# Kernel optimization log

Hardware: AMD Instinct MI355X
Metric: run time of the kernel (lower is better)

## Reference

```python
import jax, jax.numpy as jnp
import numpy as np

D_MODEL = 1024
D_STATE = 64


def setup_inputs() -> dict:
    key = jax.random.key(0)
    k_x, k_a, k_b, k_c, k_d = jax.random.split(key, 5)
    x = jax.random.normal(k_x, (4, 4096, D_MODEL), dtype=jnp.float32)
    # parameter init mirrors _init_parameters
    A_diag = jax.random.uniform(k_a, (D_STATE,), minval=-0.5, maxval=0.5, dtype=jnp.float32)
    def xavier(k, shape):
        fan_in, fan_out = shape
        limit = float(np.sqrt(6.0 / (fan_in + fan_out)))
        return jax.random.uniform(k, shape, minval=-limit, maxval=limit, dtype=jnp.float32)
    B = xavier(k_b, (D_MODEL, D_STATE))
    C = xavier(k_c, (D_STATE, D_MODEL))
    D = xavier(k_d, (D_MODEL, D_MODEL)) * 0.1
    return {"x": x, "A_diag": A_diag, "B": B, "C": C, "D": D}


def reference(x, A_diag, B, C, D):
    # h_t = sigmoid(A_diag) * h_{t-1} + x_t @ B ; y_t = h_t @ C + x_t @ D
    # dropout is identity in eval mode.
    a = jax.nn.sigmoid(A_diag)                      # [S_state]
    u = jnp.einsum('btd,ds->bts', x, B)             # precompute input drive [B,T,S]

    def step(h, u_t):                               # h: [B,S], u_t: [B,S]
        h = a * h + u_t
        return h, h

    h0 = jnp.zeros((x.shape[0], A_diag.shape[0]), dtype=x.dtype)
    _, hs = jax.lax.scan(step, h0, jnp.swapaxes(u, 0, 1))  # hs: [T,B,S]
    hs = jnp.swapaxes(hs, 0, 1)                            # [B,T,S]
    y = jnp.einsum('bts,sd->btd', hs, C) + jnp.einsum('btd,de->bte', x, D)
    return y
```

## Files before the change

### kernel.cpp

```cpp
#include <hip/hip_runtime.h>
#include <hip/hip_bf16.h>

using bf16x8 = __attribute__((ext_vector_type(8))) __bf16;
using f32x4  = __attribute__((ext_vector_type(4))) float;

#define MTOT   16384
#define DMODEL 1024
#define DSTATE 64
#define KBIG   1088

__device__ __forceinline__ ushort f2b(float f) {
  __hip_bfloat16 h = __float2bfloat16(f);
  return *reinterpret_cast<ushort*>(&h);
}

__device__ __forceinline__ void gld_lds16(const ushort* g, const char* l) {
  using gptr_t = const __attribute__((address_space(1))) uint32_t*;
  using lptr_t = __attribute__((address_space(3))) uint32_t*;
  __builtin_amdgcn_global_load_lds(
      reinterpret_cast<gptr_t>(reinterpret_cast<uintptr_t>(g)),
      reinterpret_cast<lptr_t>(static_cast<uint32_t>(reinterpret_cast<uintptr_t>(l))),
      16, 0, 0);
}

#define BARRIER() do { asm volatile("" ::: "memory"); __builtin_amdgcn_s_barrier(); asm volatile("" ::: "memory"); } while (0)
#define VMCNT4() asm volatile("s_waitcnt vmcnt(4)" ::: "memory")
#define VMCNT0() asm volatile("s_waitcnt vmcnt(0)" ::: "memory")

__global__ void prep_params(const float* __restrict__ A_diag, const float* __restrict__ B,
                            const float* __restrict__ C, const float* __restrict__ D,
                            ushort* __restrict__ Wt, ushort* __restrict__ Btu,
                            float* __restrict__ aSig) {
  int i = blockIdx.x * blockDim.x + threadIdx.x;
  int stride = gridDim.x * blockDim.x;
  for (int idx = i; idx < DMODEL * KBIG; idx += stride) {
    int n = idx / KBIG, k = idx % KBIG;
    float v = (k < DSTATE) ? C[k * DMODEL + n] : D[(size_t)(k - DSTATE) * DMODEL + n];
    Wt[idx] = f2b(v);
  }
  for (int idx = i; idx < DSTATE * DMODEL; idx += stride) {
    int s = idx >> 10, k = idx & 1023;
    Btu[idx] = f2b(B[k * DSTATE + s]);
  }
  if (i < DSTATE) aSig[i] = 1.0f / (1.0f + expf(-A_diag[i]));
}

__global__ __launch_bounds__(256) void fused_xu(const float* __restrict__ x,
    const ushort* __restrict__ Btu, const float* __restrict__ aSig,
    ushort* __restrict__ Z, float* __restrict__ Uloc, float* __restrict__ carry) {
  __shared__ ushort As[64][136];
  __shared__ float  Ul[64][68];
  int tid = threadIdx.x;
  int w = tid >> 6, lane = tid & 63;
  int l16 = lane & 15, lh = lane >> 4;
  int row0 = blockIdx.x * 64;

  f32x4 acc[4] = {};
  float4 xv[4][2];
#pragma unroll
  for (int p = 0; p < 4; ++p) {
    int fi = p * 256 + tid;
    int r = fi >> 4, kq = fi & 15;
    const float* src = x + (size_t)(row0 + r) * 1024 + kq * 8;
    xv[p][0] = *reinterpret_cast<const float4*>(src);
    xv[p][1] = *reinterpret_cast<const float4*>(src + 4);
  }
  for (int c = 0; c < 8; ++c) {
    int k0 = c * 128;
#pragma unroll
    for (int p = 0; p < 4; ++p) {
      int fi = p * 256 + tid;
      int r = fi >> 4, kq = fi & 15;
      ushort o[8] = {f2b(xv[p][0].x), f2b(xv[p][0].y), f2b(xv[p][0].z), f2b(xv[p][0].w),
                     f2b(xv[p][1].x), f2b(xv[p][1].y), f2b(xv[p][1].z), f2b(xv[p][1].w)};
      uint4 pk = *reinterpret_cast<uint4*>(o);
      *reinterpret_cast<uint4*>(&Z[(size_t)(row0 + r) * KBIG + DSTATE + k0 + kq * 8]) = pk;
      *reinterpret_cast<uint4*>(&As[r][kq * 8]) = pk;
    }
    __syncthreads();
    if (c < 7) {
      int k1 = k0 + 128;
#pragma unroll
      for (int p = 0; p < 4; ++p) {
        int fi = p * 256 + tid;
        int r = fi >> 4, kq = fi & 15;
        const float* src = x + (size_t)(row0 + r) * 1024 + k1 + kq * 8;
        xv[p][0] = *reinterpret_cast<const float4*>(src);
        xv[p][1] = *reinterpret_cast<const float4*>(src + 4);
      }
    }
#pragma unroll
    for (int ks = 0; ks < 4; ++ks) {
      bf16x8 af = *reinterpret_cast<const bf16x8*>(&As[w * 16 + l16][ks * 32 + lh * 8]);
#pragma unroll
      for (int n = 0; n < 4; ++n) {
        bf16x8 bf = *reinterpret_cast<const bf16x8*>(
            &Btu[(size_t)(n * 16 + l16) * 1024 + k0 + ks * 32 + lh * 8]);
        acc[n] = __builtin_amdgcn_mfma_f32_16x16x32_bf16(af, bf, acc[n], 0, 0, 0);
      }
    }
    __syncthreads();
  }
#pragma unroll
  for (int n = 0; n < 4; ++n)
#pragma unroll
    for (int j = 0; j < 4; ++j)
      Ul[w * 16 + lh * 4 + j][n * 16 + l16] = acc[n][j];
  __syncthreads();
  int s = lane;
  float as = aSig[s];
  float h = 0.0f;
  int g = blockIdx.x * 4 + w;
#pragma unroll
  for (int i = 0; i < 16; ++i) {
    h = fmaf(as, h, Ul[w * 16 + i][s]);
    Uloc[(size_t)(g * 16 + i) * 64 + s] = h;
  }
  carry[(size_t)g * 64 + s] = h;
}

__global__ __launch_bounds__(256) void carry_scan(const float* __restrict__ aSig,
    const float* __restrict__ carry, float* __restrict__ Hpref) {
  int b = threadIdx.x >> 6, s = threadIdx.x & 63;
  float as = aSig[s];
  float aL = as;
#pragma unroll
  for (int q = 0; q < 4; ++q) aL *= aL;
  const float* cb = carry + ((size_t)b * 256) * 64 + s;
  float* hp = Hpref + ((size_t)b * 256) * 64 + s;
  float H = 0.0f;
  for (int c0 = 0; c0 < 256; c0 += 16) {
    float v[16];
#pragma unroll
    for (int i = 0; i < 16; ++i) v[i] = cb[(size_t)(c0 + i) * 64];
#pragma unroll
    for (int i = 0; i < 16; ++i) {
      hp[(size_t)(c0 + i) * 64] = H;
      H = fmaf(aL, H, v[i]);
    }
  }
}

__global__ __launch_bounds__(256) void scan_fix2(const float* __restrict__ aSig,
    const float* __restrict__ Uloc, const float* __restrict__ Hpref,
    ushort* __restrict__ Z) {
  int w = threadIdx.x >> 6, s = threadIdx.x & 63;
  int g = blockIdx.x * 4 + w;
  float as = aSig[s];
  float H = Hpref[(size_t)g * 64 + s];
  float p = as;
  size_t ubase = (size_t)g * 16 * 64 + s;
  size_t zbase = (size_t)(g * 16) * KBIG + s;
#pragma unroll
  for (int i = 0; i < 16; ++i) {
    float h = fmaf(p, H, Uloc[ubase + (size_t)i * 64]);
    p *= as;
    Z[zbase + (size_t)i * KBIG] = f2b(h);
  }
}

__global__ __launch_bounds__(512) void gemm256(const ushort* __restrict__ A, int lda,
                                               const ushort* __restrict__ Bt, int ldb,
                                               float* __restrict__ Cc, int ldc, int K) {
  extern __shared__ __align__(128) char smem[];
  const int tid = threadIdx.x;
  const int wid = tid >> 6, lane = tid & 63;
  const int wm = wid >> 2, wn = wid & 3;
  const int l16 = lane & 15, lh = lane >> 4;

  int bid = blockIdx.x;
  int swz = (bid & 7) * ((int)gridDim.x >> 3) + (bid >> 3);
  const int bmRow = (swz >> 2) * 256;
  const int bnCol = (swz & 3) * 256;

  const int NT = K / 64;

  const int cswz = ((lh ^ (l16 & 7)) << 4);
  const int sRow = lane >> 3;
  const int sCol = (((lane & 7) ^ (lane >> 3)) << 3);

  f32x4 acc[8][4] = {};
  bf16x8 aR[8], bR[8];

  auto stageA = [&](int buf, int t, int h) {
    size_t r = (size_t)(bmRow + h * 128 + wid * 8 + sRow);
    const ushort* g0 = A + r * (size_t)lda + t * 64 + sCol;
    const char* d = smem + buf * 65536 + (h * 128 + wid * 8) * 128;
    gld_lds16(g0, d);
    gld_lds16(g0 + (size_t)64 * lda, d + 64 * 128);
  };
  auto stageB = [&](int buf, int t, int h) {
    size_t r = (size_t)(bnCol + h * 128 + wid * 8 + sRow);
    const ushort* g0 = Bt + r * (size_t)ldb + t * 64 + sCol;
    const char* d = smem + buf * 65536 + 32768 + (h * 128 + wid * 8) * 128;
    gld_lds16(g0, d);
    gld_lds16(g0 + (size_t)64 * ldb, d + 64 * 128);
  };
  auto loadA = [&](int buf, int qm) {
#pragma unroll
    for (int m = 0; m < 4; ++m)
#pragma unroll
      for (int ks = 0; ks < 2; ++ks)
        aR[m * 2 + ks] = *reinterpret_cast<const bf16x8*>(
            smem + buf * 65536 + (wm * 128 + qm * 64 + m * 16 + l16) * 128 + (cswz ^ (ks * 64)));
  };
  auto loadB = [&](int buf, int qn) {
#pragma unroll
    for (int n = 0; n < 2; ++n)
#pragma unroll
      for (int ks = 0; ks < 2; ++ks)
        bR[qn * 4 + n * 2 + ks] = *reinterpret_cast<const bf16x8*>(
            smem + buf * 65536 + 32768 + (wn * 64 + qn * 32 + n * 16 + l16) * 128 + (cswz ^ (ks * 64)));
  };
  auto mfmaQ = [&](int qm, int qn) {
    __builtin_amdgcn_s_setprio(1);
    __builtin_amdgcn_sched_barrier(0);
#pragma unroll
    for (int ks = 0; ks < 2; ++ks)
#pragma unroll
      for (int m = 0; m < 4; ++m)
#pragma unroll
        for (int n = 0; n < 2; ++n)
          acc[qm * 4 + m][qn * 2 + n] = __builtin_amdgcn_mfma_f32_16x16x32_bf16(
              aR[m * 2 + ks], bR[qn * 4 + n * 2 + ks], acc[qm * 4 + m][qn * 2 + n], 0, 0, 0);
    __builtin_amdgcn_sched_barrier(0);
    __builtin_amdgcn_s_setprio(0);
  };

  stageA(0, 0, 0); stageA(0, 0, 1); stageB(0, 0, 0); stageB(0, 0, 1);
  if (1 < NT) { stageA(1, 1, 0); stageA(1, 1, 1); stageB(1, 1, 0); stageB(1, 1, 1); }
  VMCNT0();
  BARRIER();

  for (int t = 0; t < NT; t += 2) {
    const bool s01 = (t > 0) && (t + 1 < NT);
    const bool s23 = (t + 2 < NT);
    const bool s67 = (t + 3 < NT);
    loadA(0, 0); loadB(0, 0);
    if (s01) stageA(1, t + 1, 0);
    BARRIER(); mfmaQ(0, 0); BARRIER();
    loadB(0, 1);
    if (s01) stageA(1, t + 1, 1);
    BARRIER(); mfmaQ(0, 1); BARRIER();
    loadA(0, 1);
    if (s23) stageB(0, t + 2, 0);
    BARRIER(); mfmaQ(1, 0); BARRIER();
    if (s23) stageB(0, t + 2, 1);
    BARRIER(); mfmaQ(1, 1);
    if (s23) { VMCNT4(); } else { VMCNT0(); }
    BARRIER();
    if (t + 1 < NT) {
      loadA(1, 0); loadB(1, 0);
      if (s23) stageA(0, t + 2, 0);
      BARRIER(); mfmaQ(0, 0); BARRIER();
      loadB(1, 1);
      if (s23) stageA(0, t + 2, 1);
      BARRIER(); mfmaQ(0, 1); BARRIER();
      loadA(1, 1);
      if (s67) stageB(1, t + 3, 0);
      BARRIER(); mfmaQ(1, 0); BARRIER();
      if (s67) stageB(1, t + 3, 1);
      BARRIER(); mfmaQ(1, 1);
      if (s67) { VMCNT4(); } else { VMCNT0(); }
      BARRIER();
    }
  }

#pragma unroll
  for (int i = 0; i < 8; ++i)
#pragma unroll
    for (int jn = 0; jn < 4; ++jn)
#pragma unroll
      for (int j = 0; j < 4; ++j) {
        int r = bmRow + wm * 128 + (i >> 2) * 64 + (i & 3) * 16 + lh * 4 + j;
        int c = bnCol + wn * 64 + (jn >> 1) * 32 + (jn & 1) * 16 + l16;
        Cc[(size_t)r * ldc + c] = acc[i][jn][j];
      }
}

extern "C" void kernel_launch(void* const* d_in, const int* in_sizes, int n_in,
                              void* d_out, int out_size, void* d_ws, size_t ws_size,
                              hipStream_t stream) {
  const float* x      = (const float*)d_in[0];
  const float* A_diag = (const float*)d_in[1];
  const float* B      = (const float*)d_in[2];
  const float* C      = (const float*)d_in[3];
  const float* D      = (const float*)d_in[4];
  float* y = (float*)d_out;

  char* w = (char*)d_ws;
  ushort* Z     = (ushort*)(w);
  ushort* Wt    = (ushort*)(w + 35651584);
  ushort* Btu   = (ushort*)(w + 37879808);
  float*  Uloc  = (float*) (w + 38010880);
  float*  carry = (float*) (w + 42205184);
  float*  Hpref = (float*) (w + 42467328);
  float*  aSig  = (float*) (w + 42729472);

  (void)hipFuncSetAttribute(reinterpret_cast<const void*>(&gemm256),
                            hipFuncAttributeMaxDynamicSharedMemorySize, 131072);

  prep_params<<<dim3(1024), dim3(256), 0, stream>>>(A_diag, B, C, D, Wt, Btu, aSig);
  fused_xu<<<dim3(256), dim3(256), 0, stream>>>(x, Btu, aSig, Z, Uloc, carry);
  carry_scan<<<dim3(1), dim3(256), 0, stream>>>(aSig, carry, Hpref);
  scan_fix2<<<dim3(256), dim3(256), 0, stream>>>(aSig, Uloc, Hpref, Z);
  gemm256<<<dim3(64 * 4), dim3(512), 131072, stream>>>(Z, KBIG, Wt, KBIG, y, DMODEL, KBIG);
}
```

Before: 90.98 us.

## Switch GEMM to 32x32x16 MFMA with register double-buffered k-slices

Rewrites the main 256x256 GEMM inner loop to use 32x32x16 bf16 MFMA tiles instead of 16x16x32, so each wave holds 4x2 accumulators of 16 floats. LDS fragments are read into two alternating register sets, one 16-wide k-slice ahead, while the MFMAs on the other set run. Global-to-LDS staging for the next-but-one tile is issued once per tile with a vmcnt(8) wait. The larger MFMA shape needs fewer LDS reads per flop and fewer instructions. In exchange there are fewer barrier phases to overlap memory and compute, and the new LDS swizzle and epilogue mapping must be correct.

```diff
diff --git a/kernel.cpp b/kernel.cpp
--- a/kernel.cpp
+++ b/kernel.cpp
@@ -3,6 +3,7 @@
 
 using bf16x8 = __attribute__((ext_vector_type(8))) __bf16;
 using f32x4  = __attribute__((ext_vector_type(4))) float;
+using f32x16 = __attribute__((ext_vector_type(16))) float;
 
 #define MTOT   16384
 #define DMODEL 1024
@@ -24,7 +25,7 @@
 }
 
 #define BARRIER() do { asm volatile("" ::: "memory"); __builtin_amdgcn_s_barrier(); asm volatile("" ::: "memory"); } while (0)
-#define VMCNT4() asm volatile("s_waitcnt vmcnt(4)" ::: "memory")
+#define VMCNT8() asm volatile("s_waitcnt vmcnt(8)" ::: "memory")
 #define VMCNT0() asm volatile("s_waitcnt vmcnt(0)" ::: "memory")
 
 __global__ void prep_params(const float* __restrict__ A_diag, const float* __restrict__ B,
@@ -166,115 +167,101 @@
   const int tid = threadIdx.x;
   const int wid = tid >> 6, lane = tid & 63;
   const int wm = wid >> 2, wn = wid & 3;
-  const int l16 = lane & 15, lh = lane >> 4;
+  const int l32 = lane & 31, kh = lane >> 5;
 
   int bid = blockIdx.x;
   int swz = (bid & 7) * ((int)gridDim.x >> 3) + (bid >> 3);
   const int bmRow = (swz >> 2) * 256;
   const int bnCol = (swz & 3) * 256;
-
   const int NT = K / 64;
 
-  const int cswz = ((lh ^ (l16 & 7)) << 4);
   const int sRow = lane >> 3;
   const int sCol = (((lane & 7) ^ (lane >> 3)) << 3);
 
-  f32x4 acc[8][4] = {};
-  bf16x8 aR[8], bR[8];
+  const ushort* aBase = A + (size_t)(bmRow + wid * 8 + sRow) * lda + sCol;
+  const ushort* bBase = Bt + (size_t)(bnCol + wid * 8 + sRow) * ldb + sCol;
+  char* aDst0 = smem + (wid * 8) * 128;
+  char* bDst0 = smem + 32768 + (wid * 8) * 128;
+
+  const int aRB = (wm * 128 + l32) * 128 + ((kh ^ (l32 & 7)) << 4);
+  const int bRB = 32768 + (wn * 64 + l32) * 128 + ((kh ^ (l32 & 7)) << 4);
+
+  f32x16 acc[4][2] = {};
+  bf16x8 aC[4], bC[2], aN[4], bN[2];
 
   auto stageA = [&](int buf, int t, int h) {
-    size_t r = (size_t)(bmRow + h * 128 + wid * 8 + sRow);
-    const ushort* g0 = A + r * (size_t)lda + t * 64 + sCol;
-    const char* d = smem + buf * 65536 + (h * 128 + wid * 8) * 128;
+    const ushort* g0 = aBase + (size_t)(h * 128) * lda + (size_t)t * 64;
+    const char* d = aDst0 + buf + h * 128 * 128;
     gld_lds16(g0, d);
     gld_lds16(g0 + (size_t)64 * lda, d + 64 * 128);
   };
   auto stageB = [&](int buf, int t, int h) {
-    size_t r = (size_t)(bnCol + h * 128 + wid * 8 + sRow);
-    const ushort* g0 = Bt + r * (size_t)ldb + t * 64 + sCol;
-    const char* d = smem + buf * 65536 + 32768 + (h * 128 + wid * 8) * 128;
+    const ushort* g0 = bBase + (size_t)(h * 128) * ldb + (size_t)t * 64;
+    const char* d = bDst0 + buf + h * 128 * 128;
     gld_lds16(g0, d);
     gld_lds16(g0 + (size_t)64 * ldb, d + 64 * 128);
   };
-  auto loadA = [&](int buf, int qm) {
-#pragma unroll
-    for (int m = 0; m < 4; ++m)
-#pragma unroll
-      for (int ks = 0; ks < 2; ++ks)
-        aR[m * 2 + ks] = *reinterpret_cast<const bf16x8*>(
-            smem + buf * 65536 + (wm * 128 + qm * 64 + m * 16 + l16) * 128 + (cswz ^ (ks * 64)));
-  };
-  auto loadB = [&](int buf, int qn) {
-#pragma unroll
-    for (int n = 0; n < 2; ++n)
-#pragma unroll
-      for (int ks = 0; ks < 2; ++ks)
-        bR[qn * 4 + n * 2 + ks] = *reinterpret_cast<const bf16x8*>(
-            smem + buf * 65536 + 32768 + (wn * 64 + qn * 32 + n * 16 + l16) * 128 + (cswz ^ (ks * 64)));
-  };
-  auto mfmaQ = [&](int qm, int qn) {
+  auto readA = [&](bf16x8 (&d)[4], int buf, int ks) {
+#pragma unroll
+    for (int mb = 0; mb < 4; ++mb)
+      d[mb] = *reinterpret_cast<const bf16x8*>(smem + buf + ((aRB + mb * 4096) ^ (ks << 5)));
+  };
+  auto readB = [&](bf16x8 (&d)[2], int buf, int ks) {
+#pragma unroll
+    for (int qn = 0; qn < 2; ++qn)
+      d[qn] = *reinterpret_cast<const bf16x8*>(smem + buf + ((bRB + qn * 4096) ^ (ks << 5)));
+  };
+  auto mfmaC = [&](bf16x8 (&a4)[4], bf16x8 (&b2)[2]) {
     __builtin_amdgcn_s_setprio(1);
-    __builtin_amdgcn_sched_barrier(0);
-#pragma unroll
-    for (int ks = 0; ks < 2; ++ks)
-#pragma unroll
-      for (int m = 0; m < 4; ++m)
-#pragma unroll
-        for (int n = 0; n < 2; ++n)
-          acc[qm * 4 + m][qn * 2 + n] = __builtin_amdgcn_mfma_f32_16x16x32_bf16(
-              aR[m * 2 + ks], bR[qn * 4 + n * 2 + ks], acc[qm * 4 + m][qn * 2 + n], 0, 0, 0);
-    __builtin_amdgcn_sched_barrier(0);
+#pragma unroll
+    for (int mb = 0; mb < 4; ++mb)
+#pragma unroll
+      for (int qn = 0; qn < 2; ++qn)
+        acc[mb][qn] = __builtin_amdgcn_mfma_f32_32x32x16_bf16(
+            a4[mb], b2[qn], acc[mb][qn], 0, 0, 0);
     __builtin_amdgcn_s_setprio(0);
   };
 
   stageA(0, 0, 0); stageA(0, 0, 1); stageB(0, 0, 0); stageB(0, 0, 1);
-  if (1 < NT) { stageA(1, 1, 0); stageA(1, 1, 1); stageB(1, 1, 0); stageB(1, 1, 1); }
-  VMCNT0();
+  stageA(65536, 1, 0); stageA(65536, 1, 1); stageB(65536, 1, 0); stageB(65536, 1, 1);
+  VMCNT8();
   BARRIER();
-
-  for (int t = 0; t < NT; t += 2) {
-    const bool s01 = (t > 0) && (t + 1 < NT);
-    const bool s23 = (t + 2 < NT);
-    const bool s67 = (t + 3 < NT);
-    loadA(0, 0); loadB(0, 0);
-    if (s01) stageA(1, t + 1, 0);
-    BARRIER(); mfmaQ(0, 0); BARRIER();
-    loadB(0, 1);
-    if (s01) stageA(1, t + 1, 1);
-    BARRIER(); mfmaQ(0, 1); BARRIER();
-    loadA(0, 1);
-    if (s23) stageB(0, t + 2, 0);
-    BARRIER(); mfmaQ(1, 0); BARRIER();
-    if (s23) stageB(0, t + 2, 1);
-    BARRIER(); mfmaQ(1, 1);
-    if (s23) { VMCNT4(); } else { VMCNT0(); }
-    BARRIER();
-    if (t + 1 < NT) {
-      loadA(1, 0); loadB(1, 0);
-      if (s23) stageA(0, t + 2, 0);
-      BARRIER(); mfmaQ(0, 0); BARRIER();
-      loadB(1, 1);
-      if (s23) stageA(0, t + 2, 1);
-      BARRIER(); mfmaQ(0, 1); BARRIER();
-      loadA(1, 1);
-      if (s67) stageB(1, t + 3, 0);
-      BARRIER(); mfmaQ(1, 0); BARRIER();
-      if (s67) stageB(1, t + 3, 1);
-      BARRIER(); mfmaQ(1, 1);
-      if (s67) { VMCNT4(); } else { VMCNT0(); }
-      BARRIER();
-    }
-  }
-
-#pragma unroll
-  for (int i = 0; i < 8; ++i)
-#pragma unroll
-    for (int jn = 0; jn < 4; ++jn)
-#pragma unroll
-      for (int j = 0; j < 4; ++j) {
-        int r = bmRow + wm * 128 + (i >> 2) * 64 + (i & 3) * 16 + lh * 4 + j;
-        int c = bnCol + wn * 64 + (jn >> 1) * 32 + (jn & 1) * 16 + l16;
-        Cc[(size_t)r * ldc + c] = acc[i][jn][j];
+  readA(aC, 0, 0); readB(bC, 0, 0);
+
+  for (int t = 0; t < NT; ++t) {
+    const int buf = (t & 1) << 16;
+    const bool st2 = (t + 2 < NT);
+    const bool nxt = (t + 1 < NT);
+    readA(aN, buf, 1); readB(bN, buf, 1);
+    BARRIER();
+    mfmaC(aC, bC);
+    readA(aC, buf, 2); readB(bC, buf, 2);
+    BARRIER();
+    mfmaC(aN, bN);
+    readA(aN, buf, 3); readB(bN, buf, 3);
+    BARRIER();
+    mfmaC(aC, bC);
+    if (st2) {
+      stageA(buf, t + 2, 0); stageA(buf, t + 2, 1);
+      stageB(buf, t + 2, 0); stageB(buf, t + 2, 1);
+      VMCNT8();
+    } else {
+      VMCNT0();
+    }
+    BARRIER();
+    if (nxt) { readA(aC, buf ^ 65536, 0); readB(bC, buf ^ 65536, 0); }
+    mfmaC(aN, bN);
+  }
+
+#pragma unroll
+  for (int mb = 0; mb < 4; ++mb)
+#pragma unroll
+    for (int qn = 0; qn < 2; ++qn)
+#pragma unroll
+      for (int reg = 0; reg < 16; ++reg) {
+        int r = bmRow + wm * 128 + mb * 32 + (reg & 3) + 8 * (reg >> 2) + 4 * kh;
+        int c = bnCol + wn * 64 + qn * 32 + l32;
+        Cc[(size_t)r * ldc + c] = acc[mb][qn][reg];
       }
 }
 
```

New measurement: 92.06 us. No clear change (+1.2%).

## Tile-transpose weight prep, drop block barriers in xu, fold carry scan into fixup

Applied to the files above, without the earlier changes.

Weight preparation now transposes C/D and B through 64x64 shared-memory tiles with coalesced float4 reads and 16-byte bf16 writes, replacing a strided per-element gather. The fused input-projection kernel gives each wave its own 16-row slab of shared memory, so the block-wide barriers go away. The single-block carry scan kernel is removed: each fixup wave recomputes its own prefix over earlier chunk carries, which saves a serial launch at the cost of redundant reads and FMAs.

```diff
diff --git a/kernel.cpp b/kernel.cpp
--- a/kernel.cpp
+++ b/kernel.cpp
@@ -27,41 +27,77 @@
 #define VMCNT4() asm volatile("s_waitcnt vmcnt(4)" ::: "memory")
 #define VMCNT0() asm volatile("s_waitcnt vmcnt(0)" ::: "memory")
 
-__global__ void prep_params(const float* __restrict__ A_diag, const float* __restrict__ B,
-                            const float* __restrict__ C, const float* __restrict__ D,
-                            ushort* __restrict__ Wt, ushort* __restrict__ Btu,
-                            float* __restrict__ aSig) {
-  int i = blockIdx.x * blockDim.x + threadIdx.x;
-  int stride = gridDim.x * blockDim.x;
-  for (int idx = i; idx < DMODEL * KBIG; idx += stride) {
-    int n = idx / KBIG, k = idx % KBIG;
-    float v = (k < DSTATE) ? C[k * DMODEL + n] : D[(size_t)(k - DSTATE) * DMODEL + n];
-    Wt[idx] = f2b(v);
-  }
-  for (int idx = i; idx < DSTATE * DMODEL; idx += stride) {
-    int s = idx >> 10, k = idx & 1023;
-    Btu[idx] = f2b(B[k * DSTATE + s]);
-  }
-  if (i < DSTATE) aSig[i] = 1.0f / (1.0f + expf(-A_diag[i]));
+__global__ __launch_bounds__(256) void prep_wb(const float* __restrict__ A_diag,
+    const float* __restrict__ B, const float* __restrict__ C, const float* __restrict__ D,
+    ushort* __restrict__ Wt, ushort* __restrict__ Btu, float* __restrict__ aSig) {
+  __shared__ float tile[64][65];
+  int bid = blockIdx.x;
+  int tid = threadIdx.x;
+  int r = tid >> 2;
+  if (bid < 272) {
+    int bk = bid % 17, bn = bid / 17;
+    int k0 = bk * 64, n0 = bn * 64;
+    const float* srow = (k0 + r < DSTATE)
+        ? (C + (size_t)(k0 + r) * DMODEL + n0)
+        : (D + (size_t)(k0 + r - DSTATE) * DMODEL + n0);
+#pragma unroll
+    for (int it = 0; it < 4; ++it) {
+      int c4 = (tid & 3) + it * 4;
+      float4 v = *reinterpret_cast<const float4*>(srow + c4 * 4);
+      tile[r][c4 * 4 + 0] = v.x; tile[r][c4 * 4 + 1] = v.y;
+      tile[r][c4 * 4 + 2] = v.z; tile[r][c4 * 4 + 3] = v.w;
+    }
+    __syncthreads();
+#pragma unroll
+    for (int it = 0; it < 2; ++it) {
+      int gq = (tid & 3) + it * 4;
+      ushort o[8];
+#pragma unroll
+      for (int j = 0; j < 8; ++j) o[j] = f2b(tile[gq * 8 + j][r]);
+      *reinterpret_cast<uint4*>(&Wt[(size_t)(n0 + r) * KBIG + k0 + gq * 8]) =
+          *reinterpret_cast<uint4*>(o);
+    }
+  } else {
+    int k0 = (bid - 272) * 64;
+    const float* srow = B + (size_t)(k0 + r) * DSTATE;
+#pragma unroll
+    for (int it = 0; it < 4; ++it) {
+      int c4 = (tid & 3) + it * 4;
+      float4 v = *reinterpret_cast<const float4*>(srow + c4 * 4);
+      tile[r][c4 * 4 + 0] = v.x; tile[r][c4 * 4 + 1] = v.y;
+      tile[r][c4 * 4 + 2] = v.z; tile[r][c4 * 4 + 3] = v.w;
+    }
+    __syncthreads();
+#pragma unroll
+    for (int it = 0; it < 2; ++it) {
+      int gq = (tid & 3) + it * 4;
+      ushort o[8];
+#pragma unroll
+      for (int j = 0; j < 8; ++j) o[j] = f2b(tile[gq * 8 + j][r]);
+      *reinterpret_cast<uint4*>(&Btu[(size_t)r * DMODEL + k0 + gq * 8]) =
+          *reinterpret_cast<uint4*>(o);
+    }
+    if (bid == 272 && tid < DSTATE) aSig[tid] = 1.0f / (1.0f + expf(-A_diag[tid]));
+  }
 }
 
 __global__ __launch_bounds__(256) void fused_xu(const float* __restrict__ x,
     const ushort* __restrict__ Btu, const float* __restrict__ aSig,
     ushort* __restrict__ Z, float* __restrict__ Uloc, float* __restrict__ carry) {
-  __shared__ ushort As[64][136];
-  __shared__ float  Ul[64][68];
+  __shared__ ushort As[4][16][136];
+  __shared__ float  Ul[4][16][68];
   int tid = threadIdx.x;
   int w = tid >> 6, lane = tid & 63;
   int l16 = lane & 15, lh = lane >> 4;
-  int row0 = blockIdx.x * 64;
+  int row0 = blockIdx.x * 64 + w * 16;
 
   f32x4 acc[4] = {};
   float4 xv[4][2];
 #pragma unroll
   for (int p = 0; p < 4; ++p) {
-    int fi = p * 256 + tid;
-    int r = fi >> 4, kq = fi & 15;
-    const float* src = x + (size_t)(row0 + r) * 1024 + kq * 8;
+    int fi = p * 64 + lane;
+    int r = fi >> 4, g8 = fi & 15;
+    const float* src = x + (size_t)(row0 + r) * 1024 + g8 * 8;
     xv[p][0] = *reinterpret_cast<const float4*>(src);
     xv[p][1] = *reinterpret_cast<const float4*>(src + 4);
   }
@@ -69,29 +105,28 @@
     int k0 = c * 128;
 #pragma unroll
     for (int p = 0; p < 4; ++p) {
-      int fi = p * 256 + tid;
-      int r = fi >> 4, kq = fi & 15;
+      int fi = p * 64 + lane;
+      int r = fi >> 4, g8 = fi & 15;
       ushort o[8] = {f2b(xv[p][0].x), f2b(xv[p][0].y), f2b(xv[p][0].z), f2b(xv[p][0].w),
                      f2b(xv[p][1].x), f2b(xv[p][1].y), f2b(xv[p][1].z), f2b(xv[p][1].w)};
       uint4 pk = *reinterpret_cast<uint4*>(o);
-      *reinterpret_cast<uint4*>(&Z[(size_t)(row0 + r) * KBIG + DSTATE + k0 + kq * 8]) = pk;
-      *reinterpret_cast<uint4*>(&As[r][kq * 8]) = pk;
-    }
-    __syncthreads();
+      *reinterpret_cast<uint4*>(&Z[(size_t)(row0 + r) * KBIG + DSTATE + k0 + g8 * 8]) = pk;
+      *reinterpret_cast<uint4*>(&As[w][r][g8 * 8]) = pk;
+    }
     if (c < 7) {
       int k1 = k0 + 128;
 #pragma unroll
       for (int p = 0; p < 4; ++p) {
-        int fi = p * 256 + tid;
-        int r = fi >> 4, kq = fi & 15;
-        const float* src = x + (size_t)(row0 + r) * 1024 + k1 + kq * 8;
+        int fi = p * 64 + lane;
+        int r = fi >> 4, g8 = fi & 15;
+        const float* src = x + (size_t)(row0 + r) * 1024 + k1 + g8 * 8;
         xv[p][0] = *reinterpret_cast<const float4*>(src);
         xv[p][1] = *reinterpret_cast<const float4*>(src + 4);
       }
     }
 #pragma unroll
     for (int ks = 0; ks < 4; ++ks) {
-      bf16x8 af = *reinterpret_cast<const bf16x8*>(&As[w * 16 + l16][ks * 32 + lh * 8]);
+      bf16x8 af = *reinterpret_cast<const bf16x8*>(&As[w][l16][ks * 32 + lh * 8]);
 #pragma unroll
       for (int n = 0; n < 4; ++n) {
         bf16x8 bf = *reinterpret_cast<const bf16x8*>(
@@ -99,55 +134,45 @@
         acc[n] = __builtin_amdgcn_mfma_f32_16x16x32_bf16(af, bf, acc[n], 0, 0, 0);
       }
     }
-    __syncthreads();
   }
 #pragma unroll
   for (int n = 0; n < 4; ++n)
 #pragma unroll
     for (int j = 0; j < 4; ++j)
-      Ul[w * 16 + lh * 4 + j][n * 16 + l16] = acc[n][j];
-  __syncthreads();
+      Ul[w][lh * 4 + j][n * 16 + l16] = acc[n][j];
   int s = lane;
   float as = aSig[s];
   float h = 0.0f;
   int g = blockIdx.x * 4 + w;
 #pragma unroll
   for (int i = 0; i < 16; ++i) {
-    h = fmaf(as, h, Ul[w * 16 + i][s]);
+    h = fmaf(as, h, Ul[w][i][s]);
     Uloc[(size_t)(g * 16 + i) * 64 + s] = h;
   }
   carry[(size_t)g * 64 + s] = h;
 }
 
-__global__ __launch_bounds__(256) void carry_scan(const float* __restrict__ aSig,
-    const float* __restrict__ carry, float* __restrict__ Hpref) {
-  int b = threadIdx.x >> 6, s = threadIdx.x & 63;
-  float as = aSig[s];
-  float aL = as;
-#pragma unroll
-  for (int q = 0; q < 4; ++q) aL *= aL;
-  const float* cb = carry + ((size_t)b * 256) * 64 + s;
-  float* hp = Hpref + ((size_t)b * 256) * 64 + s;
-  float H = 0.0f;
-  for (int c0 = 0; c0 < 256; c0 += 16) {
-    float v[16];
-#pragma unroll
-    for (int i = 0; i < 16; ++i) v[i] = cb[(size_t)(c0 + i) * 64];
-#pragma unroll
-    for (int i = 0; i < 16; ++i) {
-      hp[(size_t)(c0 + i) * 64] = H;
-      H = fmaf(aL, H, v[i]);
-    }
-  }
-}
-
 __global__ __launch_bounds__(256) void scan_fix2(const float* __restrict__ aSig,
-    const float* __restrict__ Uloc, const float* __restrict__ Hpref,
+    const float* __restrict__ Uloc, const float* __restrict__ carry,
     ushort* __restrict__ Z) {
   int w = threadIdx.x >> 6, s = threadIdx.x & 63;
   int g = blockIdx.x * 4 + w;
+  int b = g >> 8, c = g & 255;
   float as = aSig[s];
-  float H = Hpref[(size_t)g * 64 + s];
+  float aL = as;
+#pragma unroll
+  for (int q = 0; q < 4; ++q) aL *= aL;
+  const float* cb = carry + ((size_t)b << 8) * 64 + s;
+  float H = 0.0f;
+  for (int c0 = 0; c0 < 256; c0 += 16) {
+    if (c0 >= c) break;
+    float v[16];
+#pragma unroll
+    for (int i = 0; i < 16; ++i) v[i] = cb[(size_t)(c0 + i) * 64];
+#pragma unroll
+    for (int i = 0; i < 16; ++i)
+      if (c0 + i < c) H = fmaf(aL, H, v[i]);
+  }
   float p = as;
   size_t ubase = (size_t)g * 16 * 64 + s;
   size_t zbase = (size_t)(g * 16) * KBIG + s;
@@ -294,15 +319,13 @@
   ushort* Btu   = (ushort*)(w + 37879808);
   float*  Uloc  = (float*) (w + 38010880);
   float*  carry = (float*) (w + 42205184);
-  float*  Hpref = (float*) (w + 42467328);
-  float*  aSig  = (float*) (w + 42729472);
+  float*  aSig  = (float*) (w + 42467328);
 
   (void)hipFuncSetAttribute(reinterpret_cast<const void*>(&gemm256),
                             hipFuncAttributeMaxDynamicSharedMemorySize, 131072);
 
-  prep_params<<<dim3(1024), dim3(256), 0, stream>>>(A_diag, B, C, D, Wt, Btu, aSig);
+  prep_wb<<<dim3(288), dim3(256), 0, stream>>>(A_diag, B, C, D, Wt, Btu, aSig);
   fused_xu<<<dim3(256), dim3(256), 0, stream>>>(x, Btu, aSig, Z, Uloc, carry);
-  carry_scan<<<dim3(1), dim3(256), 0, stream>>>(aSig, carry, Hpref);
-  scan_fix2<<<dim3(256), dim3(256), 0, stream>>>(aSig, Uloc, Hpref, Z);
+  scan_fix2<<<dim3(256), dim3(256), 0, stream>>>(aSig, Uloc, carry, Z);
   gemm256<<<dim3(64 * 4), dim3(512), 131072, stream>>>(Z, KBIG, Wt, KBIG, y, DMODEL, KBIG);
 }
```

New measurement: 96.30 us. 1.06x slower.
